# Optimization experiments

Hardware: AMD Instinct MI355X
Metric: run time of the kernel (lower is better)

The kernel has to match this reference:

```python
import jax, jax.numpy as jnp
import numpy as np

N = 100000      # nodes
E = 50000       # hyperedges
NNZ = 1600000   # nonzeros in incidence matrix (avg 16 nodes/hyperedge)
C = 128         # in_channels
H = 256         # hidden_size


def setup_inputs() -> dict:
    key = jax.random.key(0)
    ks = jax.random.split(key, 8)
    x = jax.random.normal(ks[0], (N, C), dtype=jnp.float32)
    inc_rows = jax.random.randint(ks[1], (NNZ,), 0, E, dtype=jnp.int32)
    inc_cols = jax.random.randint(ks[2], (NNZ,), 0, N, dtype=jnp.int32)
    inc_vals = jax.random.uniform(ks[3], (NNZ,), dtype=jnp.float32)
    y = jax.random.randint(ks[4], (N,), 0, 10, dtype=jnp.int32)
    batch_0 = jnp.zeros((N,), dtype=jnp.int32)
    # Linear params (PyTorch Linear: y = x @ W.T + b; we store W pre-transposed as [C,H])
    s = 1.0 / np.sqrt(C)
    W0 = jax.random.uniform(ks[5], (C, H), dtype=jnp.float32, minval=-s, maxval=s)
    b0 = jnp.zeros((H,), dtype=jnp.float32)
    W1 = jax.random.uniform(ks[6], (C, H), dtype=jnp.float32, minval=-s, maxval=s)
    b1 = jnp.zeros((H,), dtype=jnp.float32)
    return {"x": x, "inc_rows": inc_rows, "inc_cols": inc_cols, "inc_vals": inc_vals,
            "y": y, "batch_0": batch_0, "W0": W0, "b0": b0, "W1": W1, "b1": b1}


def reference(x, inc_rows, inc_cols, inc_vals, y, batch_0, W0, b0, W1, b1):
    # sparse incidence @ x : gather node features per nnz, scale, scatter-add into hyperedges
    gathered = x[inc_cols] * inc_vals[:, None]                     # [NNZ, C]
    x1 = jax.ops.segment_sum(gathered, inc_rows, num_segments=E)   # [E, C]
    x0_out = jax.nn.relu(x @ W0 + b0)    # [N, H]
    x1_out = jax.nn.relu(x1 @ W1 + b1)   # [E, H]
    return (y, batch_0, x0_out, x1_out)
```

## Files before the change

### kernel.cpp

```cpp
#include <hip/hip_runtime.h>

#define N_NODES 100000
#define E_EDGES 50000
#define NNZ_CNT 1600000
#define C_IN 128
#define H_OUT 256
#define BKT 128
#define NB 391
#define RPB 4096

typedef __attribute__((ext_vector_type(8))) short short8;
typedef __attribute__((ext_vector_type(4))) float f32x4;

__device__ __forceinline__ ushort f2b(float f) {
  union { float f; uint u; } v; v.f = f;
  return (ushort)((v.u + 0x7FFFu + ((v.u >> 16) & 1u)) >> 16);
}
__device__ __forceinline__ float b2f(ushort u) {
  union { uint u; float f; } v; v.u = ((uint)u) << 16;
  return v.f;
}

__global__ __launch_bounds__(256) void init_kernel(
    const float* __restrict__ x, const int* __restrict__ y,
    const int* __restrict__ batch0, ushort* __restrict__ xb,
    float* __restrict__ out, int nconv4) {
  int i = blockIdx.x * 256 + threadIdx.x;
  if (i < nconv4) {
    float4 v = ((const float4*)x)[i];
    ushort4 u;
    u.x = f2b(v.x); u.y = f2b(v.y); u.z = f2b(v.z); u.w = f2b(v.w);
    ((ushort4*)xb)[i] = u;
  }
  if (i < N_NODES) {
    out[i]           = (float)y[i];
    out[N_NODES + i] = (float)batch0[i];
  }
}

__global__ __launch_bounds__(256) void histc_kernel(
    const int* __restrict__ rows, int* __restrict__ chist) {
  __shared__ int h[NB];
  int t = threadIdx.x;
  for (int b = t; b < NB; b += 256) h[b] = 0;
  __syncthreads();
  int i0 = blockIdx.x * RPB;
  for (int k = 0; k < RPB / 256; ++k) {
    int i = i0 + k * 256 + t;
    if (i < NNZ_CNT) atomicAdd(&h[rows[i] >> 7], 1);
  }
  __syncthreads();
  for (int b = t; b < NB; b += 256)
    if (h[b]) atomicAdd(&chist[b], h[b]);
}

__global__ __launch_bounds__(512) void scanc_kernel(
    const int* __restrict__ chist, int* __restrict__ boff,
    int* __restrict__ gtail, int* __restrict__ eoff) {
  __shared__ int s[512];
  int t = threadIdx.x;
  int v = (t < NB) ? chist[t] : 0;
  s[t] = v;
  __syncthreads();
  for (int d = 1; d < 512; d <<= 1) {
    int u = (t >= d) ? s[t - d] : 0;
    __syncthreads();
    s[t] += u;
    __syncthreads();
  }
  if (t < NB) {
    int ex = s[t] - v;
    boff[t]  = ex;
    gtail[t] = ex;
  }
  if (t == 0) { boff[NB] = NNZ_CNT; eoff[NB * BKT] = NNZ_CNT; }
}

__global__ __launch_bounds__(256) void binpass_kernel(
    const int* __restrict__ rows, const int* __restrict__ cols,
    const float* __restrict__ vals, int* __restrict__ gtail,
    uint2* __restrict__ buf) {
  __shared__ int hist[NB], rnk[NB], base[NB];
  int rcache[RPB / 256];
  int t = threadIdx.x;
  for (int b = t; b < NB; b += 256) { hist[b] = 0; rnk[b] = 0; }
  __syncthreads();
  int i0 = blockIdx.x * RPB;
#pragma unroll
  for (int k = 0; k < RPB / 256; ++k) {
    int i = i0 + k * 256 + t;
    int r = (i < NNZ_CNT) ? rows[i] : -1;
    rcache[k] = r;
    if (r >= 0) atomicAdd(&hist[r >> 7], 1);
  }
  __syncthreads();
  for (int b = t; b < NB; b += 256) {
    int c = hist[b];
    base[b] = c ? atomicAdd(&gtail[b], c) : 0;
  }
  __syncthreads();
#pragma unroll
  for (int k = 0; k < RPB / 256; ++k) {
    int r = rcache[k];
    if (r >= 0) {
      int i = i0 + k * 256 + t;
      int b = r >> 7;
      int pos = base[b] + atomicAdd(&rnk[b], 1);
      buf[pos] = make_uint2(((uint)(r & (BKT - 1)) << 17) | (uint)cols[i],
                            __float_as_uint(vals[i]));
    }
  }
}

__global__ __launch_bounds__(256) void finepass_kernel(
    const uint2* __restrict__ buf, const int* __restrict__ boff,
    uint2* __restrict__ buf2, int* __restrict__ eoff) {
  __shared__ int lhist[BKT], lexc[BKT], lrnk[BKT];
  int t = threadIdx.x;
  int b = blockIdx.x;
  if (t < BKT) { lhist[t] = 0; lrnk[t] = 0; }
  __syncthreads();
  int start = boff[b], end = boff[b + 1];
  for (int i = start + t; i < end; i += 256)
    atomicAdd(&lhist[buf[i].x >> 17], 1);
  __syncthreads();
  if (t < BKT) lexc[t] = lhist[t];
  __syncthreads();
  for (int d = 1; d < BKT; d <<= 1) {
    int v = (t < BKT && t >= d) ? lexc[t - d] : 0;
    __syncthreads();
    if (t < BKT) lexc[t] += v;
    __syncthreads();
  }
  if (t < BKT) {
    int ex = lexc[t] - lhist[t];
    lexc[t] = ex;
    eoff[b * BKT + t] = start + ex;
  }
  __syncthreads();
  for (int i = start + t; i < end; i += 256) {
    uint2 rec = buf[i];
    int rl = rec.x >> 17;
    int r = atomicAdd(&lrnk[rl], 1);
    buf2[start + lexc[rl] + r] =
        make_uint2((rec.x & 0x1FFFFu) << 8, rec.y);
  }
}

__global__ __launch_bounds__(128) void edge_reduce(
    const ushort* __restrict__ xb, const uint2* __restrict__ buf2,
    const int* __restrict__ eoff, ushort* __restrict__ x1b) {
  __shared__ uint2 meta[128];
  __shared__ float pa[2][64], pb[2][64];
  int t = threadIdx.x, wave = t >> 6, lane = t & 63;
  int e = blockIdx.x;
  int start = eoff[e], end = eoff[e + 1];
  const char* xbase = (const char*)xb + 4 * lane;
  float s00 = 0.f, s01 = 0.f, s10 = 0.f, s11 = 0.f;
  for (int base = start; base < end; base += 128) {
    int m = min(128, end - base);
    if (t < m) meta[t] = buf2[base + t];
    __syncthreads();
    int j = wave;
    for (; j + 6 < m; j += 8) {
      uint2 r0 = meta[j], r1 = meta[j + 2], r2 = meta[j + 4], r3 = meta[j + 6];
      ushort2 v0 = *(const ushort2*)(xbase + r0.x);
      ushort2 v1 = *(const ushort2*)(xbase + r1.x);
      ushort2 v2 = *(const ushort2*)(xbase + r2.x);
      ushort2 v3 = *(const ushort2*)(xbase + r3.x);
      float w0 = __uint_as_float(r0.y), w1 = __uint_as_float(r1.y);
      float w2 = __uint_as_float(r2.y), w3 = __uint_as_float(r3.y);
      s00 = fmaf(b2f(v0.x), w0, s00); s01 = fmaf(b2f(v0.y), w0, s01);
      s10 = fmaf(b2f(v1.x), w1, s10); s11 = fmaf(b2f(v1.y), w1, s11);
      s00 = fmaf(b2f(v2.x), w2, s00); s01 = fmaf(b2f(v2.y), w2, s01);
      s10 = fmaf(b2f(v3.x), w3, s10); s11 = fmaf(b2f(v3.y), w3, s11);
    }
    for (; j < m; j += 2) {
      uint2 rec = meta[j];
      float w = __uint_as_float(rec.y);
      ushort2 xv = *(const ushort2*)(xbase + rec.x);
      s00 = fmaf(b2f(xv.x), w, s00);
      s01 = fmaf(b2f(xv.y), w, s01);
    }
    __syncthreads();
  }
  pa[wave][lane] = s00 + s10;
  pb[wave][lane] = s01 + s11;
  __syncthreads();
  if (t < 64) {
    uint lo = f2b(pa[0][t] + pa[1][t]);
    uint hi = f2b(pb[0][t] + pb[1][t]);
    ((uint*)x1b)[(size_t)e * 64 + t] = lo | (hi << 16);
  }
}

__global__ __launch_bounds__(256) void wprep_kernel(
    const float* __restrict__ W0, const float* __restrict__ W1,
    ushort* __restrict__ Wf) {
  int idx = blockIdx.x * 256 + threadIdx.x;
  if (idx >= 8192) return;
  const float* W = (idx & 4096) ? W1 : W0;
  int slot = idx & 4095;
  int nt = slot >> 8, ks = (slot >> 6) & 3, lane = slot & 63;
  int c  = nt * 16 + (lane & 15);
  int kb = ks * 32 + ((lane >> 4) << 3);
  short8 v;
#pragma unroll
  for (int j = 0; j < 8; ++j) v[j] = (short)f2b(W[(kb + j) * H_OUT + c]);
  ((short8*)Wf)[idx] = v;
}

__device__ __forceinline__ void gemm_body(
    const ushort* __restrict__ A, const ushort* __restrict__ Wf,
    const float* __restrict__ bias, float* __restrict__ out, int M, int bid) {
  int wave = threadIdx.x >> 6;
  int lane = threadIdx.x & 63;
  int wm = wave >> 1, wn = wave & 1;
  int r0 = bid * 64 + wm * 32;

  int arow = lane & 15;
  int kgrp = lane >> 4;

  short8 a[2][4];
#pragma unroll
  for (int mt = 0; mt < 2; ++mt) {
    int row = min(r0 + mt * 16 + arow, M - 1);
    const ushort* ap = A + (size_t)row * C_IN + kgrp * 8;
#pragma unroll
    for (int ks = 0; ks < 4; ++ks)
      a[mt][ks] = *(const short8*)(ap + ks * 32);
  }

  f32x4 acc[2][8];
#pragma unroll
  for (int mt = 0; mt < 2; ++mt)
#pragma unroll
    for (int nt = 0; nt < 8; ++nt) acc[mt][nt] = (f32x4){0.f, 0.f, 0.f, 0.f};

#pragma unroll
  for (int nt = 0; nt < 8; ++nt) {
    int gnt = wn * 8 + nt;
    const short8* bp = (const short8*)Wf + (size_t)(gnt * 4) * 64 + lane;
#pragma unroll
    for (int ks = 0; ks < 4; ++ks) {
      short8 bfrag = bp[(size_t)ks * 64];
      acc[0][nt] = __builtin_amdgcn_mfma_f32_16x16x32_bf16(a[0][ks], bfrag, acc[0][nt], 0, 0, 0);
      acc[1][nt] = __builtin_amdgcn_mfma_f32_16x16x32_bf16(a[1][ks], bfrag, acc[1][nt], 0, 0, 0);
    }
  }

  int crow = kgrp * 4;
  int ccol = lane & 15;
#pragma unroll
  for (int mt = 0; mt < 2; ++mt) {
#pragma unroll
    for (int nt = 0; nt < 8; ++nt) {
      int col = wn * 128 + nt * 16 + ccol;
      float bb = bias[col];
#pragma unroll
      for (int reg = 0; reg < 4; ++reg) {
        int row = r0 + mt * 16 + crow + reg;
        if (row < M)
          out[(size_t)row * H_OUT + col] = fmaxf(acc[mt][nt][reg] + bb, 0.f);
      }
    }
  }
}

__global__ __launch_bounds__(256) void gemm_dual(
    const ushort* __restrict__ A0, const ushort* __restrict__ A1,
    const ushort* __restrict__ Wf, const float* __restrict__ bias0,
    const float* __restrict__ bias1, float* __restrict__ out0,
    float* __restrict__ out1, int nb0) {
  int bid = blockIdx.x;
  if (bid < nb0)
    gemm_body(A0, Wf, bias0, out0, N_NODES, bid);
  else
    gemm_body(A1, Wf + 8 * 4096, bias1, out1, E_EDGES, bid - nb0);
}

extern "C" void kernel_launch(void* const* d_in, const int* in_sizes, int n_in,
                              void* d_out, int out_size, void* d_ws, size_t ws_size,
                              hipStream_t stream) {
  const float* x        = (const float*)d_in[0];
  const int*   inc_rows = (const int*)d_in[1];
  const int*   inc_cols = (const int*)d_in[2];
  const float* inc_vals = (const float*)d_in[3];
  const int*   y        = (const int*)d_in[4];
  const int*   batch0   = (const int*)d_in[5];
  const float* W0       = (const float*)d_in[6];
  const float* b0       = (const float*)d_in[7];
  const float* W1       = (const float*)d_in[8];
  const float* b1       = (const float*)d_in[9];

  float* out = (float*)d_out;

  char* ws = (char*)d_ws;
  ushort* xb    = (ushort*)ws;  ws += (size_t)N_NODES * C_IN * 2;
  ushort* x1b   = (ushort*)ws;  ws += (size_t)E_EDGES * C_IN * 2;
  uint2*  buf   = (uint2*)ws;   ws += (size_t)NNZ_CNT * 8;
  uint2*  buf2  = (uint2*)ws;   ws += (size_t)NNZ_CNT * 8;
  ushort* Wf    = (ushort*)ws;  ws += (size_t)8192 * 8 * 2;
  int*    chist = (int*)ws;     ws += (size_t)NB * 4;
  int*    boff  = (int*)ws;     ws += (size_t)(NB + 1) * 4;
  int*    gtail = (int*)ws;     ws += (size_t)NB * 4;
  int*    eoff  = (int*)ws;

  const int nconv4 = N_NODES * C_IN / 4;
  const int nbin   = (NNZ_CNT + RPB - 1) / RPB;
  const int nb0    = (N_NODES + 63) / 64;
  const int nb1    = (E_EDGES + 63) / 64;

  wprep_kernel<<<32, 256, 0, stream>>>(W0, W1, Wf);
  hipMemsetAsync(chist, 0, (size_t)NB * 4, stream);
  init_kernel<<<(nconv4 + 255) / 256, 256, 0, stream>>>(x, y, batch0, xb, out,
                                                        nconv4);
  histc_kernel<<<nbin, 256, 0, stream>>>(inc_rows, chist);
  scanc_kernel<<<1, 512, 0, stream>>>(chist, boff, gtail, eoff);
  binpass_kernel<<<nbin, 256, 0, stream>>>(inc_rows, inc_cols, inc_vals,
                                           gtail, buf);
  finepass_kernel<<<NB, 256, 0, stream>>>(buf, boff, buf2, eoff);
  edge_reduce<<<E_EDGES, 128, 0, stream>>>(xb, buf2, eoff, x1b);

  float* x0_out = out + 2 * N_NODES;
  float* x1_out = out + 2 * N_NODES + (size_t)N_NODES * H_OUT;

  gemm_dual<<<nb0 + nb1, 256, 0, stream>>>(xb, x1b, Wf, b0, b1,
                                           x0_out, x1_out, nb0);
}
```

Measured before the change: 216.7 us.

## Fuse prep kernels and overlap node GEMM with binning passes

Merges the weight prep, bf16 conversion and row histogram into one launch. It then splits the node-feature GEMM into two halves that share launches with the coarse binning pass and the fine binning pass, so the latency-bound sort stages overlap with MFMA work. The edge GEMM becomes its own kernel after edge_reduce. This cuts launch count and idle gaps between stages, but the fused kernels carry the larger register and LDS footprint of both roles, which may lower occupancy.

```diff
diff --git a/kernel.cpp b/kernel.cpp
--- a/kernel.cpp
+++ b/kernel.cpp
@@ -8,6 +8,9 @@
 #define BKT 128
 #define NB 391
 #define RPB 4096
+#define NBIN 391
+#define GB_A 781
+#define GB_B 782
 
 typedef __attribute__((ext_vector_type(8))) short short8;
 typedef __attribute__((ext_vector_type(4))) float f32x4;
@@ -21,37 +24,107 @@
   return v.f;
 }
 
-__global__ __launch_bounds__(256) void init_kernel(
+__device__ __forceinline__ void gemm_body(
+    const ushort* __restrict__ A, const ushort* __restrict__ Wf,
+    const float* __restrict__ bias, float* __restrict__ out, int M, int bid) {
+  int wave = threadIdx.x >> 6;
+  int lane = threadIdx.x & 63;
+  int wm = wave >> 1, wn = wave & 1;
+  int r0 = bid * 64 + wm * 32;
+
+  int arow = lane & 15;
+  int kgrp = lane >> 4;
+
+  short8 a[2][4];
+#pragma unroll
+  for (int mt = 0; mt < 2; ++mt) {
+    int row = min(r0 + mt * 16 + arow, M - 1);
+    const ushort* ap = A + (size_t)row * C_IN + kgrp * 8;
+#pragma unroll
+    for (int ks = 0; ks < 4; ++ks)
+      a[mt][ks] = *(const short8*)(ap + ks * 32);
+  }
+
+  f32x4 acc[2][8];
+#pragma unroll
+  for (int mt = 0; mt < 2; ++mt)
+#pragma unroll
+    for (int nt = 0; nt < 8; ++nt) acc[mt][nt] = (f32x4){0.f, 0.f, 0.f, 0.f};
+
+#pragma unroll
+  for (int nt = 0; nt < 8; ++nt) {
+    int gnt = wn * 8 + nt;
+    const short8* bp = (const short8*)Wf + (size_t)(gnt * 4) * 64 + lane;
+#pragma unroll
+    for (int ks = 0; ks < 4; ++ks) {
+      short8 bfrag = bp[(size_t)ks * 64];
+      acc[0][nt] = __builtin_amdgcn_mfma_f32_16x16x32_bf16(a[0][ks], bfrag, acc[0][nt], 0, 0, 0);
+      acc[1][nt] = __builtin_amdgcn_mfma_f32_16x16x32_bf16(a[1][ks], bfrag, acc[1][nt], 0, 0, 0);
+    }
+  }
+
+  int crow = kgrp * 4;
+  int ccol = lane & 15;
+#pragma unroll
+  for (int mt = 0; mt < 2; ++mt) {
+#pragma unroll
+    for (int nt = 0; nt < 8; ++nt) {
+      int col = wn * 128 + nt * 16 + ccol;
+      float bb = bias[col];
+#pragma unroll
+      for (int reg = 0; reg < 4; ++reg) {
+        int row = r0 + mt * 16 + crow + reg;
+        if (row < M)
+          out[(size_t)row * H_OUT + col] = fmaxf(acc[mt][nt][reg] + bb, 0.f);
+      }
+    }
+  }
+}
+
+__global__ __launch_bounds__(256) void fused_prep(
     const float* __restrict__ x, const int* __restrict__ y,
-    const int* __restrict__ batch0, ushort* __restrict__ xb,
-    float* __restrict__ out, int nconv4) {
-  int i = blockIdx.x * 256 + threadIdx.x;
-  if (i < nconv4) {
-    float4 v = ((const float4*)x)[i];
-    ushort4 u;
-    u.x = f2b(v.x); u.y = f2b(v.y); u.z = f2b(v.z); u.w = f2b(v.w);
-    ((ushort4*)xb)[i] = u;
-  }
-  if (i < N_NODES) {
-    out[i]           = (float)y[i];
-    out[N_NODES + i] = (float)batch0[i];
-  }
-}
-
-__global__ __launch_bounds__(256) void histc_kernel(
-    const int* __restrict__ rows, int* __restrict__ chist) {
+    const int* __restrict__ batch0, const int* __restrict__ rows,
+    const float* __restrict__ W0, const float* __restrict__ W1,
+    ushort* __restrict__ xb, float* __restrict__ out,
+    int* __restrict__ chist, ushort* __restrict__ Wf, int nconv4) {
   __shared__ int h[NB];
+  int bid = blockIdx.x;
   int t = threadIdx.x;
-  for (int b = t; b < NB; b += 256) h[b] = 0;
-  __syncthreads();
-  int i0 = blockIdx.x * RPB;
-  for (int k = 0; k < RPB / 256; ++k) {
-    int i = i0 + k * 256 + t;
-    if (i < NNZ_CNT) atomicAdd(&h[rows[i] >> 7], 1);
-  }
-  __syncthreads();
-  for (int b = t; b < NB; b += 256)
-    if (h[b]) atomicAdd(&chist[b], h[b]);
+  if (bid < NBIN) {
+    for (int b = t; b < NB; b += 256) h[b] = 0;
+    __syncthreads();
+    int i0 = bid * RPB;
+    for (int k = 0; k < RPB / 256; ++k) {
+      int i = i0 + k * 256 + t;
+      if (i < NNZ_CNT) atomicAdd(&h[rows[i] >> 7], 1);
+    }
+    __syncthreads();
+    for (int b = t; b < NB; b += 256)
+      if (h[b]) atomicAdd(&chist[b], h[b]);
+  } else if (bid < NBIN + 32) {
+    int idx = (bid - NBIN) * 256 + t;
+    const float* W = (idx & 4096) ? W1 : W0;
+    int slot = idx & 4095;
+    int nt = slot >> 8, ks = (slot >> 6) & 3, lane = slot & 63;
+    int c  = nt * 16 + (lane & 15);
+    int kb = ks * 32 + ((lane >> 4) << 3);
+    short8 v;
+#pragma unroll
+    for (int j = 0; j < 8; ++j) v[j] = (short)f2b(W[(kb + j) * H_OUT + c]);
+    ((short8*)Wf)[idx] = v;
+  } else {
+    int i = (bid - NBIN - 32) * 256 + t;
+    if (i < nconv4) {
+      float4 v = ((const float4*)x)[i];
+      ushort4 u;
+      u.x = f2b(v.x); u.y = f2b(v.y); u.z = f2b(v.z); u.w = f2b(v.w);
+      ((ushort4*)xb)[i] = u;
+    }
+    if (i < N_NODES) {
+      out[i]           = (float)y[i];
+      out[N_NODES + i] = (float)batch0[i];
+    }
+  }
 }
 
 __global__ __launch_bounds__(512) void scanc_kernel(
@@ -76,16 +149,15 @@
   if (t == 0) { boff[NB] = NNZ_CNT; eoff[NB * BKT] = NNZ_CNT; }
 }
 
-__global__ __launch_bounds__(256) void binpass_kernel(
+__device__ __forceinline__ void binpass_body(
     const int* __restrict__ rows, const int* __restrict__ cols,
     const float* __restrict__ vals, int* __restrict__ gtail,
-    uint2* __restrict__ buf) {
-  __shared__ int hist[NB], rnk[NB], base[NB];
+    uint2* __restrict__ buf, int* hist, int* rnk, int* base, int bid) {
   int rcache[RPB / 256];
   int t = threadIdx.x;
   for (int b = t; b < NB; b += 256) { hist[b] = 0; rnk[b] = 0; }
   __syncthreads();
-  int i0 = blockIdx.x * RPB;
+  int i0 = bid * RPB;
 #pragma unroll
   for (int k = 0; k < RPB / 256; ++k) {
     int i = i0 + k * 256 + t;
@@ -112,12 +184,25 @@
   }
 }
 
-__global__ __launch_bounds__(256) void finepass_kernel(
+__global__ __launch_bounds__(256) void binpass_gemmA(
+    const int* __restrict__ rows, const int* __restrict__ cols,
+    const float* __restrict__ vals, int* __restrict__ gtail,
+    uint2* __restrict__ buf, const ushort* __restrict__ xb,
+    const ushort* __restrict__ Wf, const float* __restrict__ bias0,
+    float* __restrict__ out0) {
+  __shared__ int hist[NB], rnk[NB], base[NB];
+  int bid = blockIdx.x;
+  if (bid < NB)
+    binpass_body(rows, cols, vals, gtail, buf, hist, rnk, base, bid);
+  else
+    gemm_body(xb, Wf, bias0, out0, N_NODES, bid - NB);
+}
+
+__device__ __forceinline__ void finepass_body(
     const uint2* __restrict__ buf, const int* __restrict__ boff,
-    uint2* __restrict__ buf2, int* __restrict__ eoff) {
-  __shared__ int lhist[BKT], lexc[BKT], lrnk[BKT];
+    uint2* __restrict__ buf2, int* __restrict__ eoff,
+    int* lhist, int* lexc, int* lrnk, int b) {
   int t = threadIdx.x;
-  int b = blockIdx.x;
   if (t < BKT) { lhist[t] = 0; lrnk[t] = 0; }
   __syncthreads();
   int start = boff[b], end = boff[b + 1];
@@ -145,6 +230,19 @@
     buf2[start + lexc[rl] + r] =
         make_uint2((rec.x & 0x1FFFFu) << 8, rec.y);
   }
+}
+
+__global__ __launch_bounds__(256) void finepass_gemmB(
+    const uint2* __restrict__ buf, const int* __restrict__ boff,
+    uint2* __restrict__ buf2, int* __restrict__ eoff,
+    const ushort* __restrict__ xb, const ushort* __restrict__ Wf,
+    const float* __restrict__ bias0, float* __restrict__ out0) {
+  __shared__ int lhist[BKT], lexc[BKT], lrnk[BKT];
+  int bid = blockIdx.x;
+  if (bid < NB)
+    finepass_body(buf, boff, buf2, eoff, lhist, lexc, lrnk, bid);
+  else
+    gemm_body(xb, Wf, bias0, out0, N_NODES, GB_A + (bid - NB));
 }
 
 __global__ __launch_bounds__(128) void edge_reduce(
@@ -194,89 +292,10 @@
   }
 }
 
-__global__ __launch_bounds__(256) void wprep_kernel(
-    const float* __restrict__ W0, const float* __restrict__ W1,
-    ushort* __restrict__ Wf) {
-  int idx = blockIdx.x * 256 + threadIdx.x;
-  if (idx >= 8192) return;
-  const float* W = (idx & 4096) ? W1 : W0;
-  int slot = idx & 4095;
-  int nt = slot >> 8, ks = (slot >> 6) & 3, lane = slot & 63;
-  int c  = nt * 16 + (lane & 15);
-  int kb = ks * 32 + ((lane >> 4) << 3);
-  short8 v;
-#pragma unroll
-  for (int j = 0; j < 8; ++j) v[j] = (short)f2b(W[(kb + j) * H_OUT + c]);
-  ((short8*)Wf)[idx] = v;
-}
-
-__device__ __forceinline__ void gemm_body(
-    const ushort* __restrict__ A, const ushort* __restrict__ Wf,
-    const float* __restrict__ bias, float* __restrict__ out, int M, int bid) {
-  int wave = threadIdx.x >> 6;
-  int lane = threadIdx.x & 63;
-  int wm = wave >> 1, wn = wave & 1;
-  int r0 = bid * 64 + wm * 32;
-
-  int arow = lane & 15;
-  int kgrp = lane >> 4;
-
-  short8 a[2][4];
-#pragma unroll
-  for (int mt = 0; mt < 2; ++mt) {
-    int row = min(r0 + mt * 16 + arow, M - 1);
-    const ushort* ap = A + (size_t)row * C_IN + kgrp * 8;
-#pragma unroll
-    for (int ks = 0; ks < 4; ++ks)
-      a[mt][ks] = *(const short8*)(ap + ks * 32);
-  }
-
-  f32x4 acc[2][8];
-#pragma unroll
-  for (int mt = 0; mt < 2; ++mt)
-#pragma unroll
-    for (int nt = 0; nt < 8; ++nt) acc[mt][nt] = (f32x4){0.f, 0.f, 0.f, 0.f};
-
-#pragma unroll
-  for (int nt = 0; nt < 8; ++nt) {
-    int gnt = wn * 8 + nt;
-    const short8* bp = (const short8*)Wf + (size_t)(gnt * 4) * 64 + lane;
-#pragma unroll
-    for (int ks = 0; ks < 4; ++ks) {
-      short8 bfrag = bp[(size_t)ks * 64];
-      acc[0][nt] = __builtin_amdgcn_mfma_f32_16x16x32_bf16(a[0][ks], bfrag, acc[0][nt], 0, 0, 0);
-      acc[1][nt] = __builtin_amdgcn_mfma_f32_16x16x32_bf16(a[1][ks], bfrag, acc[1][nt], 0, 0, 0);
-    }
-  }
-
-  int crow = kgrp * 4;
-  int ccol = lane & 15;
-#pragma unroll
-  for (int mt = 0; mt < 2; ++mt) {
-#pragma unroll
-    for (int nt = 0; nt < 8; ++nt) {
-      int col = wn * 128 + nt * 16 + ccol;
-      float bb = bias[col];
-#pragma unroll
-      for (int reg = 0; reg < 4; ++reg) {
-        int row = r0 + mt * 16 + crow + reg;
-        if (row < M)
-          out[(size_t)row * H_OUT + col] = fmaxf(acc[mt][nt][reg] + bb, 0.f);
-      }
-    }
-  }
-}
-
-__global__ __launch_bounds__(256) void gemm_dual(
-    const ushort* __restrict__ A0, const ushort* __restrict__ A1,
-    const ushort* __restrict__ Wf, const float* __restrict__ bias0,
-    const float* __restrict__ bias1, float* __restrict__ out0,
-    float* __restrict__ out1, int nb0) {
-  int bid = blockIdx.x;
-  if (bid < nb0)
-    gemm_body(A0, Wf, bias0, out0, N_NODES, bid);
-  else
-    gemm_body(A1, Wf + 8 * 4096, bias1, out1, E_EDGES, bid - nb0);
+__global__ __launch_bounds__(256) void gemm1_kernel(
+    const ushort* __restrict__ A1, const ushort* __restrict__ Wf,
+    const float* __restrict__ bias1, float* __restrict__ out1) {
+  gemm_body(A1, Wf + 8 * 4096, bias1, out1, E_EDGES, blockIdx.x);
 }
 
 extern "C" void kernel_launch(void* const* d_in, const int* in_sizes, int n_in,
@@ -307,24 +326,20 @@
   int*    eoff  = (int*)ws;
 
   const int nconv4 = N_NODES * C_IN / 4;
-  const int nbin   = (NNZ_CNT + RPB - 1) / RPB;
-  const int nb0    = (N_NODES + 63) / 64;
+  const int ninit  = (nconv4 + 255) / 256;
   const int nb1    = (E_EDGES + 63) / 64;
-
-  wprep_kernel<<<32, 256, 0, stream>>>(W0, W1, Wf);
-  hipMemsetAsync(chist, 0, (size_t)NB * 4, stream);
-  init_kernel<<<(nconv4 + 255) / 256, 256, 0, stream>>>(x, y, batch0, xb, out,
-                                                        nconv4);
-  histc_kernel<<<nbin, 256, 0, stream>>>(inc_rows, chist);
-  scanc_kernel<<<1, 512, 0, stream>>>(chist, boff, gtail, eoff);
-  binpass_kernel<<<nbin, 256, 0, stream>>>(inc_rows, inc_cols, inc_vals,
-                                           gtail, buf);
-  finepass_kernel<<<NB, 256, 0, stream>>>(buf, boff, buf2, eoff);
-  edge_reduce<<<E_EDGES, 128, 0, stream>>>(xb, buf2, eoff, x1b);
 
   float* x0_out = out + 2 * N_NODES;
   float* x1_out = out + 2 * N_NODES + (size_t)N_NODES * H_OUT;
 
-  gemm_dual<<<nb0 + nb1, 256, 0, stream>>>(xb, x1b, Wf, b0, b1,
-                                           x0_out, x1_out, nb0);
-}
+  hipMemsetAsync(chist, 0, (size_t)NB * 4, stream);
+  fused_prep<<<NBIN + 32 + ninit, 256, 0, stream>>>(
+      x, y, batch0, inc_rows, W0, W1, xb, out, chist, Wf, nconv4);
+  scanc_kernel<<<1, 512, 0, stream>>>(chist, boff, gtail, eoff);
+  binpass_gemmA<<<NB + GB_A, 256, 0, stream>>>(
+      inc_rows, inc_cols, inc_vals, gtail, buf, xb, Wf, b0, x0_out);
+  finepass_gemmB<<<NB + GB_B, 256, 0, stream>>>(
+      buf, boff, buf2, eoff, xb, Wf, b0, x0_out);
+  edge_reduce<<<E_EDGES, 128, 0, stream>>>(xb, buf2, eoff, x1b);
+  gemm1_kernel<<<nb1, 256, 0, stream>>>(x1b, Wf, b1, x1_out);
+}
```

Result: faster. 193.3 us (median of 3 runs) (-10.8%).
